# Performance work log

Hardware: AMD Instinct MI355X
Metric: run time of the kernel (lower is better)

## Reference

```python
import jax, jax.numpy as jnp
import numpy as np

NUM_CLUSTERS = 50000
LN_EPS = 1e-5


def setup_inputs() -> dict:
    key = jax.random.key(0)
    ks = jax.random.split(key, 8)
    N, E, H = 1000000, 64, 64
    x = jax.random.normal(ks[0], (N, E), dtype=jnp.float32)
    cluster = jax.random.randint(ks[1], (N,), 0, NUM_CLUSTERS, dtype=jnp.int64)
    batch = jax.random.randint(ks[2], (N,), 0, 64, dtype=jnp.int64)
    W1 = jax.random.normal(ks[3], (E, H), dtype=jnp.float32) / np.sqrt(E)
    b1 = jnp.zeros((H,), dtype=jnp.float32)
    ln_g = jnp.ones((H,), dtype=jnp.float32)
    ln_b = jnp.zeros((H,), dtype=jnp.float32)
    W2 = jax.random.normal(ks[4], (H, E // 2), dtype=jnp.float32) / np.sqrt(H)
    b2 = jnp.zeros((E // 2,), dtype=jnp.float32)
    return {"x": x, "cluster": cluster, "batch": batch, "W1": W1, "b1": b1,
            "ln_g": ln_g, "ln_b": ln_b, "W2": W2, "b2": b2}


def _mlp(x, W1, b1, ln_g, ln_b, W2, b2):
    h = x @ W1 + b1                                   # [N, H]
    mu = jnp.mean(h, axis=-1, keepdims=True)
    var = jnp.mean(jnp.square(h - mu), axis=-1, keepdims=True)
    h = (h - mu) * jax.lax.rsqrt(var + LN_EPS) * ln_g + ln_b
    h = h * jax.nn.sigmoid(h)                         # SiLU
    return h @ W2 + b2                                # [N, E//2]


def reference(x, cluster, batch, W1, b1, ln_g, ln_b, W2, b2):
    out = _mlp(x, W1, b1, ln_g, ln_b, W2, b2)         # [N, E//2]
    cl = cluster.astype(jnp.int32)
    # max-pool per cluster (segment max), then gather back per node
    aggr = jax.ops.segment_max(out, cl, num_segments=NUM_CLUSTERS)  # [C, E//2]
    return jnp.concatenate([out, aggr[cl]], axis=-1)  # [N, E]
```

## Files before the change

### kernel.cpp

```cpp
#include <hip/hip_runtime.h>
#include <hip/hip_bf16.h>

#define NUM_CLUSTERS 50000

typedef __attribute__((ext_vector_type(8))) short bfx8;
typedef __attribute__((ext_vector_type(4))) float f32x4;

__device__ __forceinline__ unsigned fkey(float f) {
    unsigned b = __float_as_uint(f);
    return b ^ ((b & 0x80000000u) ? 0xFFFFFFFFu : 0x80000000u);
}
__device__ __forceinline__ float funkey(unsigned k) {
    unsigned b = (k & 0x80000000u) ? (k ^ 0x80000000u) : ~k;
    return __uint_as_float(b);
}
__device__ __forceinline__ unsigned short f2bf(float f) {
    unsigned u = __float_as_uint(f);
    return (unsigned short)((u + 0x7FFFu + ((u >> 16) & 1u)) >> 16);
}
__device__ __forceinline__ unsigned pk2bf(float a, float b) {
    __hip_bfloat162 h = __float22bfloat162_rn(make_float2(a, b));
    return *(unsigned*)&h;
}

__global__ __launch_bounds__(256) void prep_weights(
    const float* __restrict__ W1, const float* __restrict__ W2,
    unsigned short* __restrict__ w1f, unsigned short* __restrict__ w2f)
{
    int tid = blockIdx.x * 256 + threadIdx.x;
    if (tid < 512) {
        int frag = tid >> 6, lane = tid & 63;
        int ct = frag >> 1, kb = frag & 1;
        int col = ct * 16 + (lane & 15);
        int k0 = kb * 32 + (lane >> 4) * 8;
        #pragma unroll
        for (int i = 0; i < 8; ++i)
            w1f[(frag * 64 + lane) * 8 + i] = f2bf(W1[(k0 + i) * 64 + col]);
    } else if (tid < 768) {
        int frag = (tid - 512) >> 6, lane = tid & 63;
        int ct = frag >> 1, kb = frag & 1;
        int col = ct * 16 + (lane & 15);
        int k0 = kb * 32 + (lane >> 4) * 8;
        #pragma unroll
        for (int i = 0; i < 8; ++i)
            w2f[(frag * 64 + lane) * 8 + i] = f2bf(W2[(k0 + i) * 32 + col]);
    }
}

__global__ __launch_bounds__(256, 5) void mlp_segmax_kernel(
    const float* __restrict__ x, const int* __restrict__ cluster,
    const unsigned short* __restrict__ w1f, const float* __restrict__ b1,
    const float* __restrict__ ln_g, const float* __restrict__ ln_b,
    const unsigned short* __restrict__ w2f, const float* __restrict__ b2,
    float* __restrict__ out, unsigned* __restrict__ aggr, int N)
{
    __shared__ char smem[256 * 128];
    const int t = threadIdx.x;
    const int lane = t & 63;
    const int w = t >> 6;
    const int l15 = lane & 15;
    const int q = lane >> 4;
    const long long wbase = (long long)blockIdx.x * 256 + w * 64;
    if (wbase >= N) return;
    char* wmem = smem + w * 8192;

    #pragma unroll 4
    for (int p = 0; p < 16; ++p) {
        int le = (p * 64 + lane) * 4;
        float4 v = *(const float4*)(x + wbase * 64 + le);
        int row = le >> 6;
        int k = le & 63;
        int g = k >> 3;
        int half = (k >> 2) & 1;
        int phys = row * 128 + ((g ^ (row & 7)) << 4) + (half << 3);
        *(uint2*)(wmem + phys) = make_uint2(pk2bf(v.x, v.y), pk2bf(v.z, v.w));
    }

    bfx8 W1F[4][2], W2F[2][2];
    #pragma unroll
    for (int ct = 0; ct < 4; ++ct)
        #pragma unroll
        for (int kb = 0; kb < 2; ++kb)
            W1F[ct][kb] = *(const bfx8*)(w1f + ((ct * 2 + kb) * 64 + lane) * 8);
    #pragma unroll
    for (int ct = 0; ct < 2; ++ct)
        #pragma unroll
        for (int kb = 0; kb < 2; ++kb)
            W2F[ct][kb] = *(const bfx8*)(w2f + ((ct * 2 + kb) * 64 + lane) * 8);

    float g4[4], bb4[4], b1c[4];
    #pragma unroll
    for (int tt = 0; tt < 4; ++tt) {
        g4[tt]  = ln_g[16 * tt + l15];
        bb4[tt] = ln_b[16 * tt + l15];
        b1c[tt] = b1[16 * tt + l15];
    }
    float b2c[2] = { b2[l15], b2[16 + l15] };

    #pragma unroll 1
    for (int g = 0; g < 4; ++g) {
        const int base = g * 16;
        const int arow = base + l15;
        const int arsw = arow & 7;

        bfx8 af[2];
        #pragma unroll
        for (int kb = 0; kb < 2; ++kb)
            af[kb] = *(const bfx8*)(wmem + arow * 128 + (((kb * 4 + q) ^ arsw) << 4));

        f32x4 acc[4];
        #pragma unroll
        for (int tt = 0; tt < 4; ++tt) {
            float b = b1c[tt];
            acc[tt] = (f32x4){b, b, b, b};
        }
        #pragma unroll
        for (int kb = 0; kb < 2; ++kb)
            #pragma unroll
            for (int tt = 0; tt < 4; ++tt)
                acc[tt] = __builtin_amdgcn_mfma_f32_16x16x32_bf16(af[kb], W1F[tt][kb], acc[tt], 0, 0, 0);

        float s[4];
        #pragma unroll
        for (int r = 0; r < 4; ++r)
            s[r] = acc[0][r] + acc[1][r] + acc[2][r] + acc[3][r];
        #pragma unroll
        for (int m = 1; m < 16; m <<= 1)
            #pragma unroll
            for (int r = 0; r < 4; ++r) s[r] += __shfl_xor(s[r], m, 16);
        float mu[4];
        #pragma unroll
        for (int r = 0; r < 4; ++r) mu[r] = s[r] * (1.f / 64.f);
        float vv[4] = {0.f, 0.f, 0.f, 0.f};
        #pragma unroll
        for (int tt = 0; tt < 4; ++tt)
            #pragma unroll
            for (int r = 0; r < 4; ++r) {
                float d = acc[tt][r] - mu[r];
                vv[r] = fmaf(d, d, vv[r]);
            }
        #pragma unroll
        for (int m = 1; m < 16; m <<= 1)
            #pragma unroll
            for (int r = 0; r < 4; ++r) vv[r] += __shfl_xor(vv[r], m, 16);
        float rs[4];
        #pragma unroll
        for (int r = 0; r < 4; ++r) rs[r] = rsqrtf(vv[r] * (1.f / 64.f) + 1e-5f);

        #pragma unroll
        for (int tt = 0; tt < 4; ++tt)
            #pragma unroll
            for (int r = 0; r < 4; ++r) {
                float val = (acc[tt][r] - mu[r]) * rs[r] * g4[tt] + bb4[tt];
                val = val / (1.f + __expf(-val));
                int node = base + q * 4 + r;
                int col = 16 * tt + l15;
                int phys = node * 128 + ((((col >> 3)) ^ (node & 7)) << 4) + ((col & 7) * 2);
                *(unsigned short*)(wmem + phys) = f2bf(val);
            }

        bfx8 hf[2];
        #pragma unroll
        for (int kb = 0; kb < 2; ++kb)
            hf[kb] = *(const bfx8*)(wmem + arow * 128 + (((kb * 4 + q) ^ arsw) << 4));
        f32x4 oacc[2];
        #pragma unroll
        for (int c = 0; c < 2; ++c) {
            float b = b2c[c];
            oacc[c] = (f32x4){b, b, b, b};
        }
        #pragma unroll
        for (int kb = 0; kb < 2; ++kb)
            #pragma unroll
            for (int c = 0; c < 2; ++c)
                oacc[c] = __builtin_amdgcn_mfma_f32_16x16x32_bf16(hf[kb], W2F[c][kb], oacc[c], 0, 0, 0);

        #pragma unroll
        for (int c = 0; c < 2; ++c)
            #pragma unroll
            for (int r = 0; r < 4; ++r) {
                int node = base + q * 4 + r;
                int byte = (c * 16 + l15) * 4;
                int phys = node * 128 + (((byte >> 4) ^ (node & 7)) << 4) + (byte & 15);
                *(float*)(wmem + phys) = oacc[c][r];
            }

        int clr[4];
        #pragma unroll
        for (int r = 0; r < 4; ++r)
            clr[r] = cluster[wbase + base + q * 4 + r];
        unsigned keys[8];
        unsigned* slots[8];
        #pragma unroll
        for (int c = 0; c < 2; ++c)
            #pragma unroll
            for (int r = 0; r < 4; ++r) {
                int i = c * 4 + r;
                keys[i] = fkey(oacc[c][r]);
                slots[i] = aggr + (long long)clr[r] * 32 + c * 16 + l15;
            }
        unsigned olds[8];
        #pragma unroll
        for (int i = 0; i < 8; ++i) olds[i] = *slots[i];
        #pragma unroll
        for (int i = 0; i < 8; ++i)
            if (keys[i] > olds[i]) atomicMax(slots[i], keys[i]);
    }

    #pragma unroll 2
    for (int p = 0; p < 8; ++p) {
        int le = (p * 64 + lane) * 4;
        int row = le >> 5;
        int c = le & 31;
        f32x4 v4 = *(const f32x4*)(wmem + row * 128 + (((c >> 2) ^ (row & 7)) << 4));
        __builtin_nontemporal_store(v4, (f32x4*)(out + (wbase + row) * 64 + c));
    }
}

__global__ __launch_bounds__(256) void gather_kernel(
    const int* __restrict__ cluster, const unsigned* __restrict__ aggr,
    float* __restrict__ out, int N)
{
    long long idx = (long long)blockIdx.x * 256 + threadIdx.x;
    if (idx >= (long long)N * 8) return;
    int n = (int)(idx >> 3);
    int k4 = (int)(idx & 7) * 4;
    int c = cluster[n];
    uint4 a = *(const uint4*)(aggr + (size_t)c * 32 + k4);
    f32x4 o = {funkey(a.x), funkey(a.y), funkey(a.z), funkey(a.w)};
    __builtin_nontemporal_store(o, (f32x4*)(out + (size_t)n * 64 + 32 + k4));
}

extern "C" void kernel_launch(void* const* d_in, const int* in_sizes, int n_in,
                              void* d_out, int out_size, void* d_ws, size_t ws_size,
                              hipStream_t stream) {
    const float* x     = (const float*)d_in[0];
    const int* cluster = (const int*)d_in[1];
    const float* W1    = (const float*)d_in[3];
    const float* b1    = (const float*)d_in[4];
    const float* ln_g  = (const float*)d_in[5];
    const float* ln_b  = (const float*)d_in[6];
    const float* W2    = (const float*)d_in[7];
    const float* b2    = (const float*)d_in[8];
    float* out = (float*)d_out;

    unsigned* aggr = (unsigned*)d_ws;
    unsigned short* w1f = (unsigned short*)((char*)d_ws + (size_t)NUM_CLUSTERS * 32 * 4);
    unsigned short* w2f = w1f + 8 * 64 * 8;

    int N = in_sizes[0] / 64;

    hipMemsetAsync(aggr, 0, (size_t)NUM_CLUSTERS * 32 * sizeof(unsigned), stream);
    prep_weights<<<3, 256, 0, stream>>>(W1, W2, w1f, w2f);

    int blocks1 = (N + 255) / 256;
    mlp_segmax_kernel<<<blocks1, 256, 0, stream>>>(
        x, cluster, w1f, b1, ln_g, ln_b, w2f, b2, out, aggr, N);

    long long total2 = (long long)N * 8;
    int blocks2 = (int)((total2 + 255) / 256);
    gather_kernel<<<blocks2, 256, 0, stream>>>(cluster, aggr, out, N);
}
```

Before: 271.6 us.

## Load x directly into MFMA fragments and stream outputs per 16-row group

```diff
diff --git a/kernel.cpp b/kernel.cpp
--- a/kernel.cpp
+++ b/kernel.cpp
@@ -5,6 +5,8 @@
 
 typedef __attribute__((ext_vector_type(8))) short bfx8;
 typedef __attribute__((ext_vector_type(4))) float f32x4;
+
+union BF8 { bfx8 v; unsigned u[4]; };
 
 __device__ __forceinline__ unsigned fkey(float f) {
     unsigned b = __float_as_uint(f);
@@ -54,7 +56,7 @@
     const unsigned short* __restrict__ w2f, const float* __restrict__ b2,
     float* __restrict__ out, unsigned* __restrict__ aggr, int N)
 {
-    __shared__ char smem[256 * 128];
+    __shared__ char smem[4 * 2048];
     const int t = threadIdx.x;
     const int lane = t & 63;
     const int w = t >> 6;
@@ -62,19 +64,7 @@
     const int q = lane >> 4;
     const long long wbase = (long long)blockIdx.x * 256 + w * 64;
     if (wbase >= N) return;
-    char* wmem = smem + w * 8192;
-
-    #pragma unroll 4
-    for (int p = 0; p < 16; ++p) {
-        int le = (p * 64 + lane) * 4;
-        float4 v = *(const float4*)(x + wbase * 64 + le);
-        int row = le >> 6;
-        int k = le & 63;
-        int g = k >> 3;
-        int half = (k >> 2) & 1;
-        int phys = row * 128 + ((g ^ (row & 7)) << 4) + (half << 3);
-        *(uint2*)(wmem + phys) = make_uint2(pk2bf(v.x, v.y), pk2bf(v.z, v.w));
-    }
+    char* wmem = smem + w * 2048;
 
     bfx8 W1F[4][2], W2F[2][2];
     #pragma unroll
@@ -99,14 +89,29 @@
 
     #pragma unroll 1
     for (int g = 0; g < 4; ++g) {
-        const int base = g * 16;
-        const int arow = base + l15;
-        const int arsw = arow & 7;
-
-        bfx8 af[2];
-        #pragma unroll
-        for (int kb = 0; kb < 2; ++kb)
-            af[kb] = *(const bfx8*)(wmem + arow * 128 + (((kb * 4 + q) ^ arsw) << 4));
+        const long long gbase = wbase + g * 16;
+
+        const float* xr = x + (gbase + l15) * 64 + q * 8;
+        float4 a0 = *(const float4*)(xr);
+        float4 a1 = *(const float4*)(xr + 4);
+        float4 a2 = *(const float4*)(xr + 32);
+        float4 a3 = *(const float4*)(xr + 36);
+
+        int clr[4];
+        #pragma unroll
+        for (int r = 0; r < 4; ++r) clr[r] = cluster[gbase + q * 4 + r];
+        unsigned olds[8];
+        #pragma unroll
+        for (int c2 = 0; c2 < 2; ++c2)
+            #pragma unroll
+            for (int r = 0; r < 4; ++r)
+                olds[c2 * 4 + r] = aggr[(long long)clr[r] * 32 + c2 * 16 + l15];
+
+        BF8 af0, af1;
+        af0.u[0] = pk2bf(a0.x, a0.y); af0.u[1] = pk2bf(a0.z, a0.w);
+        af0.u[2] = pk2bf(a1.x, a1.y); af0.u[3] = pk2bf(a1.z, a1.w);
+        af1.u[0] = pk2bf(a2.x, a2.y); af1.u[1] = pk2bf(a2.z, a2.w);
+        af1.u[2] = pk2bf(a3.x, a3.y); af1.u[3] = pk2bf(a3.z, a3.w);
 
         f32x4 acc[4];
         #pragma unroll
@@ -115,10 +120,11 @@
             acc[tt] = (f32x4){b, b, b, b};
         }
         #pragma unroll
-        for (int kb = 0; kb < 2; ++kb)
-            #pragma unroll
-            for (int tt = 0; tt < 4; ++tt)
-                acc[tt] = __builtin_amdgcn_mfma_f32_16x16x32_bf16(af[kb], W1F[tt][kb], acc[tt], 0, 0, 0);
+        for (int tt = 0; tt < 4; ++tt)
+            acc[tt] = __builtin_amdgcn_mfma_f32_16x16x32_bf16(af0.v, W1F[tt][0], acc[tt], 0, 0, 0);
+        #pragma unroll
+        for (int tt = 0; tt < 4; ++tt)
+            acc[tt] = __builtin_amdgcn_mfma_f32_16x16x32_bf16(af1.v, W1F[tt][1], acc[tt], 0, 0, 0);
 
         float s[4];
         #pragma unroll
@@ -153,7 +159,7 @@
             for (int r = 0; r < 4; ++r) {
                 float val = (acc[tt][r] - mu[r]) * rs[r] * g4[tt] + bb4[tt];
                 val = val / (1.f + __expf(-val));
-                int node = base + q * 4 + r;
+                int node = q * 4 + r;
                 int col = 16 * tt + l15;
                 int phys = node * 128 + ((((col >> 3)) ^ (node & 7)) << 4) + ((col & 7) * 2);
                 *(unsigned short*)(wmem + phys) = f2bf(val);
@@ -162,58 +168,46 @@
         bfx8 hf[2];
         #pragma unroll
         for (int kb = 0; kb < 2; ++kb)
-            hf[kb] = *(const bfx8*)(wmem + arow * 128 + (((kb * 4 + q) ^ arsw) << 4));
+            hf[kb] = *(const bfx8*)(wmem + l15 * 128 + (((kb * 4 + q) ^ (l15 & 7)) << 4));
         f32x4 oacc[2];
         #pragma unroll
-        for (int c = 0; c < 2; ++c) {
-            float b = b2c[c];
-            oacc[c] = (f32x4){b, b, b, b};
+        for (int c2 = 0; c2 < 2; ++c2) {
+            float b = b2c[c2];
+            oacc[c2] = (f32x4){b, b, b, b};
         }
         #pragma unroll
         for (int kb = 0; kb < 2; ++kb)
             #pragma unroll
-            for (int c = 0; c < 2; ++c)
-                oacc[c] = __builtin_amdgcn_mfma_f32_16x16x32_bf16(hf[kb], W2F[c][kb], oacc[c], 0, 0, 0);
-
-        #pragma unroll
-        for (int c = 0; c < 2; ++c)
-            #pragma unroll
-            for (int r = 0; r < 4; ++r) {
-                int node = base + q * 4 + r;
-                int byte = (c * 16 + l15) * 4;
+            for (int c2 = 0; c2 < 2; ++c2)
+                oacc[c2] = __builtin_amdgcn_mfma_f32_16x16x32_bf16(hf[kb], W2F[c2][kb], oacc[c2], 0, 0, 0);
+
+        #pragma unroll
+        for (int c2 = 0; c2 < 2; ++c2)
+            #pragma unroll
+            for (int r = 0; r < 4; ++r) {
+                int node = q * 4 + r;
+                int byte = (c2 * 16 + l15) * 4;
                 int phys = node * 128 + (((byte >> 4) ^ (node & 7)) << 4) + (byte & 15);
-                *(float*)(wmem + phys) = oacc[c][r];
-            }
-
-        int clr[4];
-        #pragma unroll
-        for (int r = 0; r < 4; ++r)
-            clr[r] = cluster[wbase + base + q * 4 + r];
-        unsigned keys[8];
-        unsigned* slots[8];
-        #pragma unroll
-        for (int c = 0; c < 2; ++c)
-            #pragma unroll
-            for (int r = 0; r < 4; ++r) {
-                int i = c * 4 + r;
-                keys[i] = fkey(oacc[c][r]);
-                slots[i] = aggr + (long long)clr[r] * 32 + c * 16 + l15;
-            }
-        unsigned olds[8];
-        #pragma unroll
-        for (int i = 0; i < 8; ++i) olds[i] = *slots[i];
-        #pragma unroll
-        for (int i = 0; i < 8; ++i)
-            if (keys[i] > olds[i]) atomicMax(slots[i], keys[i]);
-    }
-
-    #pragma unroll 2
-    for (int p = 0; p < 8; ++p) {
-        int le = (p * 64 + lane) * 4;
-        int row = le >> 5;
-        int c = le & 31;
-        f32x4 v4 = *(const f32x4*)(wmem + row * 128 + (((c >> 2) ^ (row & 7)) << 4));
-        __builtin_nontemporal_store(v4, (f32x4*)(out + (wbase + row) * 64 + c));
+                *(float*)(wmem + phys) = oacc[c2][r];
+            }
+
+        #pragma unroll
+        for (int p = 0; p < 2; ++p) {
+            int le = (p * 64 + lane) * 4;
+            int row = le >> 5;
+            int c = le & 31;
+            f32x4 v4 = *(const f32x4*)(wmem + row * 128 + (((c >> 2) ^ (row & 7)) << 4));
+            __builtin_nontemporal_store(v4, (f32x4*)(out + (gbase + row) * 64 + c));
+        }
+
+        #pragma unroll
+        for (int c2 = 0; c2 < 2; ++c2)
+            #pragma unroll
+            for (int r = 0; r < 4; ++r) {
+                unsigned key = fkey(oacc[c2][r]);
+                if (key > olds[c2 * 4 + r])
+                    atomicMax(aggr + (long long)clr[r] * 32 + c2 * 16 + l15, key);
+            }
     }
 }
 
```

Result: slower. 367.5 us (+35.3%).
